# Kernel tuning notes

Hardware: AMD Instinct MI355X
Metric: run time of the kernel (lower is better)

## Reference

```python
import jax, jax.numpy as jnp
import numpy as np

F, H, NSEQ, T, A, LP, LV = 256, 256, 64, 2048, 32, 512, 512
N = NSEQ * T


def setup_inputs() -> dict:
    key = jax.random.key(0)
    ks = jax.random.split(key, 24)
    p = lambda k, shape: jax.random.normal(k, shape, jnp.float32) * 0.05
    return {
        'features': jax.random.normal(ks[0], (N, F), jnp.float32),
        'episode_starts': (jax.random.uniform(ks[1], (N,)) < 0.005).astype(jnp.float32),
        'h_pi': jax.random.normal(ks[2], (1, NSEQ, H), jnp.float32),
        'c_pi': jax.random.normal(ks[3], (1, NSEQ, H), jnp.float32),
        'h_vf': jax.random.normal(ks[4], (1, NSEQ, H), jnp.float32),
        'c_vf': jax.random.normal(ks[5], (1, NSEQ, H), jnp.float32),
        'W_feat': p(ks[6], (4 * F, F)), 'b_feat': jnp.zeros((4 * F,), jnp.float32),
        'W_emb': p(ks[7], (H, F)), 'b_emb': jnp.zeros((H,), jnp.float32),
        'W_ih': p(ks[8], (4 * H, F)), 'W_hh': p(ks[9], (4 * H, H)),
        'b_ih': jnp.zeros((4 * H,), jnp.float32), 'b_hh': jnp.zeros((4 * H,), jnp.float32),
        'Wp1': p(ks[10], (LP, H + 3 * F)), 'bp1': jnp.zeros((LP,), jnp.float32),
        'Wp2': p(ks[11], (A, LP)), 'bp2': jnp.zeros((A,), jnp.float32),
        'Wv1': p(ks[12], (LV, H + 3 * F)), 'bv1': jnp.zeros((LV,), jnp.float32),
        'Wv2': p(ks[13], (1, LV)), 'bv2': jnp.zeros((1,), jnp.float32),
    }


def _lstm_masked_scan(feats, starts, h0, c0, W_ih, W_hh, b_ih, b_hh):
    # feats: (T, n_seq, F), starts: (T, n_seq); PyTorch gate order i,f,g,o
    xg = jnp.einsum('tnf,gf->tng', feats, W_ih) + b_ih  # precompute input gates

    def step(carry, xs):
        h, c = carry
        xg_t, s_t = xs
        m = (1.0 - s_t)[:, None]          # episode-reset mask
        h = h * m
        c = c * m
        g = xg_t + h @ W_hh.T + b_hh
        i, f, gg, o = jnp.split(g, 4, axis=-1)
        c = jax.nn.sigmoid(f) * c + jax.nn.sigmoid(i) * jnp.tanh(gg)
        h = jax.nn.sigmoid(o) * jnp.tanh(c)
        return (h, c), h

    (hT, cT), hs = jax.lax.scan(step, (h0, c0), (xg, starts))
    return hs, hT, cT


def reference(features, episode_starts, h_pi, c_pi, h_vf, c_vf,
              W_feat, b_feat, W_emb, b_emb, W_ih, W_hh, b_ih, b_hh,
              Wp1, bp1, Wp2, bp2, Wv1, bv1, Wv2, bv2):
    n_seq = h_vf.shape[1]
    feats = features.reshape(n_seq, -1, F).swapaxes(0, 1)      # (T, n_seq, F)
    starts = episode_starts.reshape(n_seq, -1).swapaxes(0, 1)  # (T, n_seq)

    feat4 = jnp.einsum('tnf,gf->tng', feats, W_feat) + b_feat  # (T, n_seq, 4F)
    f1 = feat4[..., : 3 * F]
    f1_flat = f1.swapaxes(0, 1).reshape(-1, 3 * F)             # (N, 3F)

    # actor branch: TempLSTM ignores its LSTM -> just Linear(F, H) on raw feats;
    # the loop branch feeds raw features_sequence (source behavior).
    out_pi = jnp.einsum('tnf,hf->tnh', feats, W_emb) + b_emb   # (T, n_seq, H)
    out_pi_flat = out_pi.swapaxes(0, 1).reshape(-1, H)

    # critic branch: masked LSTM recurrence with per-step episode resets
    hs, hT, cT = _lstm_masked_scan(feats, starts, h_vf[0], c_vf[0], W_ih, W_hh, b_ih, b_hh)
    hs_flat = hs.swapaxes(0, 1).reshape(-1, H)

    latent_pi = jnp.concatenate([f1_flat, out_pi_flat], axis=-1)
    latent_vf = jnp.concatenate([f1_flat, hs_flat], axis=-1)

    values = jax.nn.relu(latent_vf @ Wv1.T + bv1) @ Wv2.T + bv2      # (N, 1)
    logits = jax.nn.relu(latent_pi @ Wp1.T + bp1) @ Wp2.T + bp2      # (N, A)

    actions = jnp.argmax(logits, axis=-1)  # deterministic=True -> mode
    log_prob = jnp.take_along_axis(jax.nn.log_softmax(logits, axis=-1), actions[:, None], axis=1)[:, 0]

    # actor final state = h0 scaled by product of reset masks (loop semantics)
    mprod = jnp.prod(1.0 - starts, axis=0)[None, :, None]
    h_pi_f, c_pi_f = h_pi * mprod, c_pi * mprod
    return actions, values, log_prob, h_pi_f, c_pi_f, hT[None], cT[None]
```

## Files before the change

### kernel.cpp

```cpp
#include <hip/hip_runtime.h>
#include <stdint.h>
#include <math.h>

#define N_TOT 131072
#define TSEQ  2048
#define NSEQ  64
#define CS    128
#define NCH   16
#define PARTS 4

typedef unsigned long long u64;

__global__ __launch_bounds__(256)
void transpose_whh(const float* __restrict__ Whh, float* __restrict__ Wg)
{
    const int k = blockIdx.x;
    const int u = threadIdx.x;
#pragma unroll
    for (int g = 0; g < 4; ++g)
        Wg[(size_t)k * 1024 + u * 4 + g] = Whh[(size_t)(g * 256 + u) * 256 + k];
}

__global__ __launch_bounds__(256)
void gemm_xg(const float* __restrict__ A, const float* __restrict__ Wih,
             const float* __restrict__ bih, const float* __restrict__ bhh,
             float* __restrict__ xg, int base)
{
    __shared__ float As[16][136];
    __shared__ float Bs[16][136];
    const int t  = threadIdx.x;
    const int n0 = blockIdx.x * 128;
    const int seq = blockIdx.y;
    const size_t grow0 = (size_t)seq * TSEQ + base;
    const size_t lrow0 = (size_t)seq * CS;
    const int tx = t & 15, ty = t >> 4;

    float acc[8][8];
#pragma unroll
    for (int i = 0; i < 8; ++i)
#pragma unroll
        for (int j = 0; j < 8; ++j) acc[i][j] = 0.f;

    for (int kt = 0; kt < 256; kt += 16) {
#pragma unroll
        for (int jj = 0; jj < 2; ++jj) {
            int idx = t + 256 * jj;
            int m = idx >> 2, q = idx & 3;
            float4 a = *(const float4*)(A + (grow0 + m) * 256 + kt + q * 4);
            As[q * 4 + 0][m] = a.x; As[q * 4 + 1][m] = a.y;
            As[q * 4 + 2][m] = a.z; As[q * 4 + 3][m] = a.w;
            float4 b = *(const float4*)(Wih + (size_t)(n0 + m) * 256 + kt + q * 4);
            Bs[q * 4 + 0][m] = b.x; Bs[q * 4 + 1][m] = b.y;
            Bs[q * 4 + 2][m] = b.z; Bs[q * 4 + 3][m] = b.w;
        }
        __syncthreads();
#pragma unroll
        for (int k = 0; k < 16; ++k) {
            float4 a0 = *(const float4*)&As[k][ty * 8];
            float4 a1 = *(const float4*)&As[k][ty * 8 + 4];
            float4 b0 = *(const float4*)&Bs[k][tx * 8];
            float4 b1 = *(const float4*)&Bs[k][tx * 8 + 4];
            float av[8] = {a0.x, a0.y, a0.z, a0.w, a1.x, a1.y, a1.z, a1.w};
            float bv[8] = {b0.x, b0.y, b0.z, b0.w, b1.x, b1.y, b1.z, b1.w};
#pragma unroll
            for (int i = 0; i < 8; ++i)
#pragma unroll
                for (int j = 0; j < 8; ++j) acc[i][j] += av[i] * bv[j];
        }
        __syncthreads();
    }
#pragma unroll
    for (int i = 0; i < 8; ++i) {
        size_t lr = lrow0 + ty * 8 + i;
#pragma unroll
        for (int j = 0; j < 8; ++j) {
            int n = n0 + tx * 8 + j;
            int gate = n >> 8, u = n & 255;
            xg[lr * 1024 + u * 4 + gate] = acc[i][j] + bih[n] + bhh[n];
        }
    }
}

__global__ __launch_bounds__(1024)
void lstm4(const float* __restrict__ xg, const float* __restrict__ starts,
           const float* __restrict__ h0g, const float* __restrict__ c0g,
           float* __restrict__ hstate, float* __restrict__ cstate,
           const float* __restrict__ Wg,
           float* __restrict__ hs, float* __restrict__ hT,
           float* __restrict__ cT,
           u64* __restrict__ hx, int base)
{
    __shared__ float hmask[256];
    __shared__ float part[16][64][4];

    const int t   = threadIdx.x;
    const int seq = blockIdx.x >> 2;
    const int p   = blockIdx.x & 3;
    const int u   = t & 63;
    const int q   = t >> 6;

    float4 Wr[16];
#pragma unroll
    for (int kk = 0; kk < 16; ++kk)
        Wr[kk] = *(const float4*)(Wg + (size_t)(q * 16 + kk) * 1024 + (p * 64 + u) * 4);

    float c_reg = 0.f;
    if (t < 64) {
        const float* csrc = (base == 0) ? c0g : cstate;
        c_reg = csrc[(size_t)seq * 256 + p * 64 + t];
    }

    for (int lt = 0; lt < CS; ++lt) {
        const int S = base + lt;
        const float m = 1.f - starts[(size_t)seq * TSEQ + S];

        float4 x4 = make_float4(0.f, 0.f, 0.f, 0.f);
        if (t < 64)
            x4 = *(const float4*)(xg + ((size_t)seq * CS + lt) * 1024 + (p * 64 + t) * 4);

        if (lt == 0) {
            if (t < 256) {
                const float* hsrc = (base == 0) ? h0g : hstate;
                hmask[t] = hsrc[(size_t)seq * 256 + t] * m;
            }
        } else {
            if (t < 256) {
                const size_t idx = (size_t)(S & 1) * (NSEQ * 256) + (size_t)seq * 256 + t;
                u64 w; unsigned spins = 0;
                for (;;) {
                    w = __hip_atomic_load(&hx[idx], __ATOMIC_RELAXED,
                                          __HIP_MEMORY_SCOPE_AGENT);
                    if ((unsigned)(w >> 32) == (unsigned)S) break;
                    __builtin_amdgcn_s_sleep(1);
                    if (++spins > (1u << 20)) break;
                }
                hmask[t] = __uint_as_float((unsigned)w) * m;
            }
        }
        __syncthreads();

        const float* hp = &hmask[q * 16];
        float4 h0 = *(const float4*)(hp + 0);
        float4 h1 = *(const float4*)(hp + 4);
        float4 h2 = *(const float4*)(hp + 8);
        float4 h3 = *(const float4*)(hp + 12);
        float hv[16] = {h0.x,h0.y,h0.z,h0.w, h1.x,h1.y,h1.z,h1.w,
                        h2.x,h2.y,h2.z,h2.w, h3.x,h3.y,h3.z,h3.w};
        float a0 = 0.f, a1 = 0.f, a2 = 0.f, a3 = 0.f;
#pragma unroll
        for (int kk = 0; kk < 16; ++kk) {
            a0 += hv[kk] * Wr[kk].x;
            a1 += hv[kk] * Wr[kk].y;
            a2 += hv[kk] * Wr[kk].z;
            a3 += hv[kk] * Wr[kk].w;
        }
        *(float4*)&part[q][u][0] = make_float4(a0, a1, a2, a3);
        __syncthreads();

        if (t < 64) {
            float gi = 0.f, gf = 0.f, gg = 0.f, go = 0.f;
#pragma unroll
            for (int qq = 0; qq < 16; ++qq) {
                float4 pp = *(const float4*)&part[qq][t][0];
                gi += pp.x; gf += pp.y; gg += pp.z; go += pp.w;
            }
            gi += x4.x; gf += x4.y; gg += x4.z; go += x4.w;
            float c = c_reg * m;
            float si = 1.f / (1.f + expf(-gi));
            float sf = 1.f / (1.f + expf(-gf));
            float so = 1.f / (1.f + expf(-go));
            c = sf * c + si * tanhf(gg);
            float h = so * tanhf(c);
            c_reg = c;

            const int gu = p * 64 + t;
            const size_t widx = (size_t)((S + 1) & 1) * (NSEQ * 256)
                              + (size_t)seq * 256 + gu;
            __hip_atomic_store(&hx[widx],
                               ((u64)(unsigned)(S + 1) << 32) |
                               (u64)__float_as_uint(h),
                               __ATOMIC_RELAXED, __HIP_MEMORY_SCOPE_AGENT);
            hs[((size_t)seq * CS + lt) * 256 + gu] = h;
            if (lt == CS - 1) {
                cstate[(size_t)seq * 256 + gu] = c;
                hstate[(size_t)seq * 256 + gu] = h;
            }
            if (S == TSEQ - 1) {
                cT[(size_t)seq * 256 + gu] = c;
                hT[(size_t)seq * 256 + gu] = h;
            }
        }
    }
}

__global__ __launch_bounds__(256)
void gemm_latent(const float* __restrict__ A, const float* __restrict__ Wfeat,
                 const float* __restrict__ Wemb, const float* __restrict__ bfeat,
                 const float* __restrict__ bemb, float* __restrict__ lat, int base)
{
    __shared__ float As[16][72];
    __shared__ float Bs[16][72];
    const int t  = threadIdx.x;
    const int n0 = blockIdx.x * 64;
    const size_t lr0 = (size_t)blockIdx.y * 64;
    const size_t grow0 = (lr0 >> 7) * TSEQ + base + (lr0 & 127);
    const int tx = t & 15, ty = t >> 4;

    double acc[4][4];
#pragma unroll
    for (int i = 0; i < 4; ++i)
#pragma unroll
        for (int j = 0; j < 4; ++j) acc[i][j] = 0.0;

    for (int kt = 0; kt < 256; kt += 16) {
        {
            int m = t >> 2, q = t & 3;
            float4 a = *(const float4*)(A + (grow0 + m) * 256 + kt + q * 4);
            As[q * 4 + 0][m] = a.x; As[q * 4 + 1][m] = a.y;
            As[q * 4 + 2][m] = a.z; As[q * 4 + 3][m] = a.w;
            int n = n0 + m;
            const float* Brow = (n < 768) ? (Wfeat + (size_t)n * 256)
                                          : (Wemb + (size_t)(n - 768) * 256);
            float4 b = *(const float4*)(Brow + kt + q * 4);
            Bs[q * 4 + 0][m] = b.x; Bs[q * 4 + 1][m] = b.y;
            Bs[q * 4 + 2][m] = b.z; Bs[q * 4 + 3][m] = b.w;
        }
        __syncthreads();
        float p[4][4];
#pragma unroll
        for (int i = 0; i < 4; ++i)
#pragma unroll
            for (int j = 0; j < 4; ++j) p[i][j] = 0.f;
#pragma unroll
        for (int k = 0; k < 16; ++k) {
            float4 a0 = *(const float4*)&As[k][ty * 4];
            float4 b0 = *(const float4*)&Bs[k][tx * 4];
            float av[4] = {a0.x, a0.y, a0.z, a0.w};
            float bv[4] = {b0.x, b0.y, b0.z, b0.w};
#pragma unroll
            for (int i = 0; i < 4; ++i)
#pragma unroll
                for (int j = 0; j < 4; ++j) p[i][j] += av[i] * bv[j];
        }
#pragma unroll
        for (int i = 0; i < 4; ++i)
#pragma unroll
            for (int j = 0; j < 4; ++j) acc[i][j] += (double)p[i][j];
        __syncthreads();
    }
#pragma unroll
    for (int i = 0; i < 4; ++i) {
        size_t lr = lr0 + ty * 4 + i;
#pragma unroll
        for (int j = 0; j < 4; ++j) {
            int n = n0 + tx * 4 + j;
            float v = (float)acc[i][j];
            v += (n < 768) ? bfeat[n] : bemb[n - 768];
            lat[lr * 1024 + n] = v;
        }
    }
}

__global__ __launch_bounds__(256)
void gemm_h1p(const float* __restrict__ lat, const float* __restrict__ Wp1,
              const float* __restrict__ bp1, float* __restrict__ h1)
{
    __shared__ float As[16][72];
    __shared__ float Bs[16][72];
    const int t  = threadIdx.x;
    const int n0 = blockIdx.x * 64;
    const size_t lr0 = (size_t)blockIdx.y * 64;
    const int tx = t & 15, ty = t >> 4;

    double acc[4][4];
#pragma unroll
    for (int i = 0; i < 4; ++i)
#pragma unroll
        for (int j = 0; j < 4; ++j) acc[i][j] = 0.0;

    for (int kt = 0; kt < 1024; kt += 16) {
        {
            int m = t >> 2, q = t & 3;
            float4 a = *(const float4*)(lat + (lr0 + m) * 1024 + kt + q * 4);
            As[q * 4 + 0][m] = a.x; As[q * 4 + 1][m] = a.y;
            As[q * 4 + 2][m] = a.z; As[q * 4 + 3][m] = a.w;
            float4 b = *(const float4*)(Wp1 + (size_t)(n0 + m) * 1024 + kt + q * 4);
            Bs[q * 4 + 0][m] = b.x; Bs[q * 4 + 1][m] = b.y;
            Bs[q * 4 + 2][m] = b.z; Bs[q * 4 + 3][m] = b.w;
        }
        __syncthreads();
        float p[4][4];
#pragma unroll
        for (int i = 0; i < 4; ++i)
#pragma unroll
            for (int j = 0; j < 4; ++j) p[i][j] = 0.f;
#pragma unroll
        for (int k = 0; k < 16; ++k) {
            float4 a0 = *(const float4*)&As[k][ty * 4];
            float4 b0 = *(const float4*)&Bs[k][tx * 4];
            float av[4] = {a0.x, a0.y, a0.z, a0.w};
            float bv[4] = {b0.x, b0.y, b0.z, b0.w};
#pragma unroll
            for (int i = 0; i < 4; ++i)
#pragma unroll
                for (int j = 0; j < 4; ++j) p[i][j] += av[i] * bv[j];
        }
#pragma unroll
        for (int i = 0; i < 4; ++i)
#pragma unroll
            for (int j = 0; j < 4; ++j) acc[i][j] += (double)p[i][j];
        __syncthreads();
    }
#pragma unroll
    for (int i = 0; i < 4; ++i) {
        size_t lr = lr0 + ty * 4 + i;
#pragma unroll
        for (int j = 0; j < 4; ++j) {
            int n = n0 + tx * 4 + j;
            float v = (float)acc[i][j] + bp1[n];
            h1[lr * 512 + n] = v > 0.f ? v : 0.f;
        }
    }
}

__global__ __launch_bounds__(256)
void gemm_h1v(const float* __restrict__ lat, const float* __restrict__ hs,
              const float* __restrict__ Wv1, const float* __restrict__ bv1,
              float* __restrict__ h1)
{
    __shared__ float As[16][136];
    __shared__ float Bs[16][136];
    const int t  = threadIdx.x;
    const int n0 = blockIdx.x * 128;
    const size_t lrow0 = (size_t)blockIdx.y * 128;
    const int tx = t & 15, ty = t >> 4;

    float acc[8][8];
#pragma unroll
    for (int i = 0; i < 8; ++i)
#pragma unroll
        for (int j = 0; j < 8; ++j) acc[i][j] = 0.f;

    for (int pass = 0; pass < 2; ++pass) {
        const float* A  = (pass == 0) ? lat : hs;
        const int lda   = (pass == 0) ? 1024 : 256;
        const int kmax  = (pass == 0) ? 768 : 256;
        const int boff  = (pass == 0) ? 0 : 768;
        for (int kt = 0; kt < kmax; kt += 16) {
#pragma unroll
            for (int jj = 0; jj < 2; ++jj) {
                int idx = t + 256 * jj;
                int m = idx >> 2, q = idx & 3;
                float4 a = *(const float4*)(A + (lrow0 + m) * lda + kt + q * 4);
                As[q * 4 + 0][m] = a.x; As[q * 4 + 1][m] = a.y;
                As[q * 4 + 2][m] = a.z; As[q * 4 + 3][m] = a.w;
                float4 b = *(const float4*)(Wv1 + (size_t)(n0 + m) * 1024 + boff + kt + q * 4);
                Bs[q * 4 + 0][m] = b.x; Bs[q * 4 + 1][m] = b.y;
                Bs[q * 4 + 2][m] = b.z; Bs[q * 4 + 3][m] = b.w;
            }
            __syncthreads();
#pragma unroll
            for (int k = 0; k < 16; ++k) {
                float4 a0 = *(const float4*)&As[k][ty * 8];
                float4 a1 = *(const float4*)&As[k][ty * 8 + 4];
                float4 b0 = *(const float4*)&Bs[k][tx * 8];
                float4 b1 = *(const float4*)&Bs[k][tx * 8 + 4];
                float av[8] = {a0.x, a0.y, a0.z, a0.w, a1.x, a1.y, a1.z, a1.w};
                float bv[8] = {b0.x, b0.y, b0.z, b0.w, b1.x, b1.y, b1.z, b1.w};
#pragma unroll
                for (int i = 0; i < 8; ++i)
#pragma unroll
                    for (int j = 0; j < 8; ++j) acc[i][j] += av[i] * bv[j];
            }
            __syncthreads();
        }
    }
#pragma unroll
    for (int i = 0; i < 8; ++i) {
        size_t lr = lrow0 + ty * 8 + i;
#pragma unroll
        for (int j = 0; j < 8; ++j) {
            int n = n0 + tx * 8 + j;
            float v = acc[i][j] + bv1[n];
            h1[lr * 512 + n] = v > 0.f ? v : 0.f;
        }
    }
}

__global__ __launch_bounds__(256)
void mask_kernel(const float* __restrict__ starts, const float* __restrict__ h_pi,
                 const float* __restrict__ c_pi,
                 float* __restrict__ o_hpi, float* __restrict__ o_cpi)
{
    __shared__ float red[256];
    const int n = blockIdx.x, t = threadIdx.x;
    float a = 0.f;
    for (int j = 0; j < 8; ++j)
        a = fmaxf(a, starts[(size_t)n * TSEQ + t * 8 + j]);
    red[t] = a; __syncthreads();
    for (int s = 128; s > 0; s >>= 1) {
        if (t < s) red[t] = fmaxf(red[t], red[t + s]);
        __syncthreads();
    }
    float m = (red[0] > 0.f) ? 0.f : 1.f;
    o_hpi[(size_t)n * 256 + t] = h_pi[(size_t)n * 256 + t] * m;
    o_cpi[(size_t)n * 256 + t] = c_pi[(size_t)n * 256 + t] * m;
}

__global__ __launch_bounds__(256)
void policy_finish(const float* __restrict__ h1p, const float* __restrict__ Wp2,
                   const float* __restrict__ bp2,
                   float* __restrict__ o_actions, float* __restrict__ o_logp,
                   int base)
{
    __shared__ float w2t[512 * 32];
    const int t = threadIdx.x;
    for (int j = 0; j < 64; ++j) {
        int idx = t + 256 * j;
        int k = idx >> 5, c = idx & 31;
        w2t[idx] = Wp2[(size_t)c * 512 + k];
    }
    __syncthreads();

    const int c = t & 31;
    size_t lr = (size_t)blockIdx.x * 8 + (t >> 5);
    size_t grow = (lr >> 7) * TSEQ + base + (lr & 127);
    const float* hrow = h1p + lr * 512;
    double s = 0.0;
    for (int k = 0; k < 512; k += 4) {
        float4 h4 = *(const float4*)(hrow + k);
        s += (double)h4.x * (double)w2t[(k + 0) * 32 + c];
        s += (double)h4.y * (double)w2t[(k + 1) * 32 + c];
        s += (double)h4.z * (double)w2t[(k + 2) * 32 + c];
        s += (double)h4.w * (double)w2t[(k + 3) * 32 + c];
    }
    double logit = s + (double)bp2[c];

    double mv = logit; int mi = c;
#pragma unroll
    for (int off = 16; off >= 1; off >>= 1) {
        double ov = __shfl_xor(mv, off, 32);
        int    oi = __shfl_xor(mi, off, 32);
        if (ov > mv || (ov == mv && oi < mi)) { mv = ov; mi = oi; }
    }
    double se = exp(logit - mv);
#pragma unroll
    for (int off = 16; off >= 1; off >>= 1) se += __shfl_xor(se, off, 32);

    if (c == 0) {
        o_actions[grow] = (float)mi;
        o_logp[grow]    = (float)(-log(se));
    }
}

__global__ __launch_bounds__(256)
void value_finish(const float* __restrict__ h1v, const float* __restrict__ Wv2,
                  const float* __restrict__ bv2, float* __restrict__ o_values,
                  int base)
{
    __shared__ float wv[512];
    const int t = threadIdx.x;
    wv[t] = Wv2[t]; wv[t + 256] = Wv2[t + 256];
    __syncthreads();
    const int q = t & 3;
    size_t lr = (size_t)blockIdx.x * 64 + (t >> 2);
    size_t grow = (lr >> 7) * TSEQ + base + (lr & 127);
    const float* hrow = h1v + lr * 512;
    float s = 0.f;
    for (int k = q * 128; k < q * 128 + 128; k += 4) {
        float4 h4 = *(const float4*)(hrow + k);
        float4 w4 = *(const float4*)&wv[k];
        s += h4.x * w4.x + h4.y * w4.y + h4.z * w4.z + h4.w * w4.w;
    }
    s += __shfl_xor(s, 1, 4);
    s += __shfl_xor(s, 2, 4);
    if (q == 0) o_values[grow] = s + bv2[0];
}

extern "C" void kernel_launch(void* const* d_in, const int* in_sizes, int n_in,
                              void* d_out, int out_size, void* d_ws, size_t ws_size,
                              hipStream_t stream)
{
    const float* features = (const float*)d_in[0];
    const float* starts   = (const float*)d_in[1];
    const float* h_pi     = (const float*)d_in[2];
    const float* c_pi     = (const float*)d_in[3];
    const float* h_vf     = (const float*)d_in[4];
    const float* c_vf     = (const float*)d_in[5];
    const float* W_feat   = (const float*)d_in[6];
    const float* b_feat   = (const float*)d_in[7];
    const float* W_emb    = (const float*)d_in[8];
    const float* b_emb    = (const float*)d_in[9];
    const float* W_ih     = (const float*)d_in[10];
    const float* W_hh     = (const float*)d_in[11];
    const float* b_ih     = (const float*)d_in[12];
    const float* b_hh     = (const float*)d_in[13];
    const float* Wp1      = (const float*)d_in[14];
    const float* bp1      = (const float*)d_in[15];
    const float* Wp2      = (const float*)d_in[16];
    const float* bp2      = (const float*)d_in[17];
    const float* Wv1      = (const float*)d_in[18];
    const float* bv1      = (const float*)d_in[19];
    const float* Wv2      = (const float*)d_in[20];
    const float* bv2      = (const float*)d_in[21];

    float* out = (float*)d_out;
    float* o_actions = out;
    float* o_values  = out + N_TOT;
    float* o_logp    = out + 2 * (size_t)N_TOT;
    float* o_hpi     = out + 3 * (size_t)N_TOT;
    float* o_cpi     = o_hpi + NSEQ * 256;
    float* o_hT      = o_cpi + NSEQ * 256;
    float* o_cT      = o_hT  + NSEQ * 256;

    char* ws = (char*)d_ws;
    const size_t MB = 1024 * 1024;
    float* xg_c  = (float*)(ws);
    float* lat_c = (float*)(ws + 32 * MB);
    float* hs_c  = (float*)(ws + 64 * MB);
    float* h1_c  = (float*)(ws + 72 * MB);
    float* Wg    = (float*)(ws + 88 * MB);
    float* hstate = (float*)(ws + 89 * MB);
    float* cstate = (float*)(ws + 89 * MB + 65536);
    u64*   hx     = (u64*)  (ws + 89 * MB + 131072);

    transpose_whh<<<256, 256, 0, stream>>>(W_hh, Wg);

    mask_kernel<<<NSEQ, 256, 0, stream>>>(starts, h_pi, c_pi, o_hpi, o_cpi);

    for (int c = 0; c < NCH; ++c) {
        const int base = c * CS;

        gemm_xg<<<dim3(8, NSEQ), 256, 0, stream>>>(features, W_ih, b_ih, b_hh,
                                                   xg_c, base);
        lstm4<<<NSEQ * PARTS, 1024, 0, stream>>>(xg_c, starts, h_vf, c_vf,
                                                 hstate, cstate, Wg,
                                                 hs_c, o_hT, o_cT, hx, base);

        gemm_latent<<<dim3(16, 128), 256, 0, stream>>>(
            features, W_feat, W_emb, b_feat, b_emb, lat_c, base);

        gemm_h1p<<<dim3(8, 128), 256, 0, stream>>>(lat_c, Wp1, bp1, h1_c);
        policy_finish<<<1024, 256, 0, stream>>>(h1_c, Wp2, bp2,
                                                o_actions, o_logp, base);

        gemm_h1v<<<dim3(4, 64), 256, 0, stream>>>(lat_c, hs_c, Wv1, bv1, h1_c);
        value_finish<<<128, 256, 0, stream>>>(h1_c, Wv2, bv2, o_values, base);
    }
}
```

Before: 16.69 ms.

## Add fast L2-coherent inline-asm handshake path for LSTM cross-block hidden exchange

Adds a second mirror buffer for the per-step hidden state exchange between the four blocks of each sequence, written with plain global stores and polled with sc0 loads via inline asm, without sleeping between polls. A global fallback flag switches every block back to the original atomic-with-sleep path if any poll times out. Block-to-sequence mapping is also remapped so the four partner blocks of a sequence get different block IDs, which may change where they are scheduled. The intent is to cut inter-block synchronization latency on each of the 2048 recurrent steps. The risks are coherence assumptions about which cache level the asm loads and stores reach, and extra store traffic from the duplicate write.

```diff
diff --git a/kernel.cpp b/kernel.cpp
--- a/kernel.cpp
+++ b/kernel.cpp
@@ -81,6 +81,21 @@
     }
 }
 
+__device__ __forceinline__ void l2_store_u64(u64* p, u64 v)
+{
+    asm volatile("global_store_dwordx2 %0, %1, off"
+                 :: "v"(p), "v"(v) : "memory");
+}
+
+__device__ __forceinline__ u64 l2_load_u64(const u64* p)
+{
+    u64 v;
+    asm volatile("global_load_dwordx2 %0, %1, off sc0\n\t"
+                 "s_waitcnt vmcnt(0)"
+                 : "=v"(v) : "v"(p) : "memory");
+    return v;
+}
+
 __global__ __launch_bounds__(1024)
 void lstm4(const float* __restrict__ xg, const float* __restrict__ starts,
            const float* __restrict__ h0g, const float* __restrict__ c0g,
@@ -88,16 +103,20 @@
            const float* __restrict__ Wg,
            float* __restrict__ hs, float* __restrict__ hT,
            float* __restrict__ cT,
-           u64* __restrict__ hx, int base)
+           u64* __restrict__ hx, u64* __restrict__ hx2,
+           unsigned* __restrict__ fastState,
+           int base, int fastflag)
 {
     __shared__ float hmask[256];
     __shared__ float part[16][64][4];
 
-    const int t   = threadIdx.x;
-    const int seq = blockIdx.x >> 2;
-    const int p   = blockIdx.x & 3;
-    const int u   = t & 63;
-    const int q   = t >> 6;
+    const int t    = threadIdx.x;
+    const int bid  = blockIdx.x;
+    const int slot = bid >> 3;
+    const int seq  = (bid & 7) + 8 * (slot >> 2);
+    const int p    = slot & 3;
+    const int u    = t & 63;
+    const int q    = t >> 6;
 
     float4 Wr[16];
 #pragma unroll
@@ -108,6 +127,13 @@
     if (t < 64) {
         const float* csrc = (base == 0) ? c0g : cstate;
         c_reg = csrc[(size_t)seq * 256 + p * 64 + t];
+    }
+
+    bool useFast = (fastflag != 0);
+    if (useFast) {
+        unsigned st = __hip_atomic_load(fastState, __ATOMIC_RELAXED,
+                                        __HIP_MEMORY_SCOPE_AGENT);
+        if (st != 0u) useFast = false;
     }
 
     for (int lt = 0; lt < CS; ++lt) {
@@ -126,13 +152,29 @@
         } else {
             if (t < 256) {
                 const size_t idx = (size_t)(S & 1) * (NSEQ * 256) + (size_t)seq * 256 + t;
-                u64 w; unsigned spins = 0;
-                for (;;) {
-                    w = __hip_atomic_load(&hx[idx], __ATOMIC_RELAXED,
-                                          __HIP_MEMORY_SCOPE_AGENT);
-                    if ((unsigned)(w >> 32) == (unsigned)S) break;
-                    __builtin_amdgcn_s_sleep(1);
-                    if (++spins > (1u << 20)) break;
+                u64 w = 0;
+                if (useFast) {
+                    int tries = 0;
+                    for (;;) {
+                        w = l2_load_u64(&hx2[idx]);
+                        if ((unsigned)(w >> 32) == (unsigned)S) break;
+                        if (++tries > 768) {
+                            useFast = false;
+                            __hip_atomic_store(fastState, 1u, __ATOMIC_RELAXED,
+                                               __HIP_MEMORY_SCOPE_AGENT);
+                            break;
+                        }
+                    }
+                }
+                if (!useFast) {
+                    unsigned spins = 0;
+                    for (;;) {
+                        w = __hip_atomic_load(&hx[idx], __ATOMIC_RELAXED,
+                                              __HIP_MEMORY_SCOPE_AGENT);
+                        if ((unsigned)(w >> 32) == (unsigned)S) break;
+                        __builtin_amdgcn_s_sleep(1);
+                        if (++spins > (1u << 18)) break;
+                    }
                 }
                 hmask[t] = __uint_as_float((unsigned)w) * m;
             }
@@ -176,9 +218,10 @@
             const int gu = p * 64 + t;
             const size_t widx = (size_t)((S + 1) & 1) * (NSEQ * 256)
                               + (size_t)seq * 256 + gu;
-            __hip_atomic_store(&hx[widx],
-                               ((u64)(unsigned)(S + 1) << 32) |
-                               (u64)__float_as_uint(h),
+            const u64 pkt = ((u64)(unsigned)(S + 1) << 32)
+                          | (u64)__float_as_uint(h);
+            if (fastflag) l2_store_u64(&hx2[widx], pkt);
+            __hip_atomic_store(&hx[widx], pkt,
                                __ATOMIC_RELAXED, __HIP_MEMORY_SCOPE_AGENT);
             hs[((size_t)seq * CS + lt) * 256 + gu] = h;
             if (lt == CS - 1) {
@@ -523,6 +566,12 @@
     float* hstate = (float*)(ws + 89 * MB);
     float* cstate = (float*)(ws + 89 * MB + 65536);
     u64*   hx     = (u64*)  (ws + 89 * MB + 131072);
+    u64*   hx2    = (u64*)  (ws + 89 * MB + 393216);
+    unsigned* fastState = (unsigned*)(ws + 89 * MB + 655360);
+
+    const int fastflag = (ws_size >= 89 * MB + 656 * 1024) ? 1 : 0;
+    u64* hx2_eff = fastflag ? hx2 : hx;
+    unsigned* fs_eff = fastflag ? fastState : (unsigned*)hx;
 
     transpose_whh<<<256, 256, 0, stream>>>(W_hh, Wg);
 
@@ -535,7 +584,8 @@
                                                    xg_c, base);
         lstm4<<<NSEQ * PARTS, 1024, 0, stream>>>(xg_c, starts, h_vf, c_vf,
                                                  hstate, cstate, Wg,
-                                                 hs_c, o_hT, o_cT, hx, base);
+                                                 hs_c, o_hT, o_cT, hx, hx2_eff,
+                                                 fs_eff, base, fastflag);
 
         gemm_latent<<<dim3(16, 128), 256, 0, stream>>>(
             features, W_feat, W_emb, b_feat, b_emb, lat_c, base);
```

Result: faster. 15.46 ms (-7.3%).
